# Kernel optimization log

Hardware: AMD Instinct MI355X
Metric: run time of the kernel (lower is better)

The kernel has to match this reference:

```python
import jax, jax.numpy as jnp
import numpy as np

N, E = 50000, 400000
HID, EDGE, NRBF = 128, 16, 32
CUTOFF = 5.0
EPS = 1e-8


def setup_inputs() -> dict:
    key = jax.random.key(0)
    ks = jax.random.split(key, 16)
    s = lambda fan_in: 1.0 / np.sqrt(fan_in)
    mlp_in = 3 * HID + NRBF + EDGE  # 432
    return {
        "h": jax.random.normal(ks[0], (N, HID), jnp.float32),
        "vec": jax.random.normal(ks[1], (N, 3, HID), jnp.float32),
        "coord": jax.random.normal(ks[2], (N, 3), jnp.float32),
        "edge_index": jax.random.randint(ks[3], (2, E), 0, N, jnp.int32),
        "edge_attr": jax.random.normal(ks[4], (E, EDGE), jnp.float32),
        "Wvp": jax.random.normal(ks[5], (HID, 3 * HID), jnp.float32) * s(HID),
        "W1": jax.random.normal(ks[6], (mlp_in, HID), jnp.float32) * s(mlp_in),
        "b1": jnp.zeros((HID,), jnp.float32),
        "W2": jax.random.normal(ks[7], (HID, HID), jnp.float32) * s(HID),
        "b2": jnp.zeros((HID,), jnp.float32),
        "W3": jax.random.normal(ks[8], (HID, 3 * HID), jnp.float32) * s(HID),
        "b3": jnp.zeros((3 * HID,), jnp.float32),
        "Wop": jax.random.normal(ks[9], (HID, 3 * HID), jnp.float32) * s(HID),
        "bop": jnp.zeros((3 * HID,), jnp.float32),
    }


def _rbf(d):
    # Gaussian smearing: centers on linspace(0, cutoff, n_rbf)
    offsets = jnp.linspace(0.0, CUTOFF, NRBF, dtype=d.dtype)
    coeff = -0.5 / (offsets[1] - offsets[0]) ** 2
    return jnp.exp(coeff * (d[:, None] - offsets) ** 2)  # [E, NRBF]


def reference(h, vec, coord, edge_index, edge_attr,
              Wvp, W1, b1, W2, b2, W3, b3, Wop, bop):
    row, col = edge_index[0], edge_index[1]
    x_ij = coord[row] - coord[col]                          # [E,3]
    d = jnp.sqrt(jnp.sum(x_ij * x_ij, axis=-1) + EPS)       # stable_norm
    d_ij = _rbf(d)                                          # [E,NRBF]

    vecp = jnp.einsum('nvh,hk->nvk', vec, Wvp)              # [N,3,3H]
    vec1, vec2, vec3 = jnp.split(vecp, 3, axis=-1)          # each [N,3,H]
    vec_dot = jnp.sum(vec1 * vec2, axis=1)                  # [N,H]

    cross = jnp.sum(vec1[row] * vec2[col], axis=1)          # [E,H]
    mlp_in = jnp.concatenate([h[row], h[col], d_ij, cross, edge_attr], axis=-1)
    x = jax.nn.silu(mlp_in @ W1 + b1)
    x = jax.nn.silu(x @ W2 + b2)
    msg = x @ W3 + b3                                       # [E,3H]
    msg_h, msg_v, msg_x = jnp.split(msg, 3, axis=1)

    h_aggr = jax.ops.segment_sum(msg_h, row, num_segments=N)           # [N,H]
    vec_msg = vec3[col] * msg_v[:, None, :] + msg_x[:, None, :] * x_ij[:, :, None]
    vec_aggr = jax.ops.segment_sum(vec_msg, row, num_segments=N)       # [N,3,H]

    o = h_aggr @ Wop + bop
    o1, o2, o3 = jnp.split(o, 3, axis=1)
    dh = vec_dot * o2 + o3
    dvec = vec3 * o1[:, None, :] + vec_aggr
    return dh, dvec
```

## Files before the change

### kernel.cpp

```cpp
#include <hip/hip_runtime.h>
#include <math.h>

constexpr int NN    = 50000;
constexpr int NE    = 400000;
constexpr int HID   = 128;

constexpr size_t OFF_VECP = 0;
constexpr size_t OFF_HAGG = 57600000;
constexpr size_t OFF_HW   = 64000000;
constexpr size_t OFF_OBUF = 64000000;
constexpr size_t OFF_WT   = 83200000;
constexpr size_t OFF_PERM = 83421184;
constexpr size_t OFF_DEG  = 83821184;
constexpr size_t OFF_CUR  = 83871184;
constexpr size_t WS_FLOATS = 83921184;

constexpr size_t O_HWH = 0;
constexpr size_t O_HWL = 32768;
constexpr size_t O_W1H = 65536;
constexpr size_t O_W1L = 90112;
constexpr size_t O_W2H = 114688;
constexpr size_t O_W2L = 131072;
constexpr size_t O_W3H = 147456;
constexpr size_t O_W3L = 196608;
constexpr size_t O_VPH = 245760;
constexpr size_t O_VPL = 294912;
constexpr size_t O_OPH = 344064;
constexpr size_t O_OPL = 393216;

typedef __attribute__((ext_vector_type(8))) short short8;
typedef __attribute__((ext_vector_type(4))) float f32x4;

__device__ __forceinline__ short f2bf_rne(float f) {
    unsigned u = __float_as_uint(f);
    u += 0x7fffu + ((u >> 16) & 1u);
    return (short)(u >> 16);
}
__device__ __forceinline__ float bf2f(short h) {
    return __uint_as_float(((unsigned)(unsigned short)h) << 16);
}
__device__ __forceinline__ void split8(const float* t, short8& ah, short8& al) {
#pragma unroll
    for (int j = 0; j < 8; ++j) {
        short hi = f2bf_rne(t[j]);
        ah[j] = hi;
        al[j] = f2bf_rne(t[j] - bf2f(hi));
    }
}
__device__ __forceinline__ f32x4 mfma3(short8 ah, short8 al, short8 bh, short8 bl, f32x4 c) {
    c = __builtin_amdgcn_mfma_f32_16x16x32_bf16(ah, bh, c, 0, 0, 0);
    c = __builtin_amdgcn_mfma_f32_16x16x32_bf16(al, bh, c, 0, 0, 0);
    c = __builtin_amdgcn_mfma_f32_16x16x32_bf16(ah, bl, c, 0, 0, 0);
    return c;
}

#define VLOAD8(dst, src) do { \
    *(float4*)&(dst)[0] = *(const float4*)(src); \
    *(float4*)&(dst)[4] = *(const float4*)((src) + 4); } while (0)

__global__ void sort_hist(const int* __restrict__ eidx, int* __restrict__ deg)
{
    int e = blockIdx.x * 256 + threadIdx.x;
    if (e < NE) atomicAdd(&deg[eidx[e]], 1);
}

__global__ void __launch_bounds__(1024)
sort_scan(const int* __restrict__ deg, int* __restrict__ cursor)
{
    __shared__ int part[1024];
    const int tid = threadIdx.x;
    const int base = tid * 49;
    int s = 0;
#pragma unroll 7
    for (int j = 0; j < 49; ++j) {
        int i = base + j;
        if (i < NN) s += deg[i];
    }
    part[tid] = s;
    __syncthreads();
    for (int off = 1; off < 1024; off <<= 1) {
        int v = (tid >= off) ? part[tid - off] : 0;
        __syncthreads();
        part[tid] += v;
        __syncthreads();
    }
    int run = part[tid] - s;
    for (int j = 0; j < 49; ++j) {
        int i = base + j;
        if (i < NN) { cursor[i] = run; run += deg[i]; }
    }
}

__global__ void sort_scatter(const int* __restrict__ eidx, int* __restrict__ cursor,
                             int* __restrict__ perm)
{
    int e = blockIdx.x * 256 + threadIdx.x;
    if (e < NE) {
        int pos = atomicAdd(&cursor[eidx[e]], 1);
        perm[pos] = e;
    }
}

__global__ void wprep_kernel(const float* __restrict__ W1, const float* __restrict__ W2,
                             const float* __restrict__ W3, const float* __restrict__ Wvp,
                             const float* __restrict__ Wop, short* __restrict__ wt)
{
    int idx = blockIdx.x * 256 + threadIdx.x;
    float v; size_t oh, ol;
    if (idx < 32768) {
        int j = idx >> 7, k = idx & 127;
        v = (j < 128) ? W1[(size_t)k * 128 + j] : W1[(size_t)(128 + k) * 128 + (j - 128)];
        oh = O_HWH + idx; ol = O_HWL + idx;
    } else if (idx < 57344) {
        int l = idx - 32768; int n = l / 192, k = l - n * 192;
        int r = (k < 128) ? (288 + k) : (k < 160) ? (256 + k - 128) : (k < 176) ? (416 + k - 160) : -1;
        v = (r < 0) ? 0.f : W1[(size_t)r * 128 + n];
        oh = O_W1H + l; ol = O_W1L + l;
    } else if (idx < 73728) {
        int l = idx - 57344; int n = l >> 7, k = l & 127;
        v = W2[(size_t)k * 128 + n];
        oh = O_W2H + l; ol = O_W2L + l;
    } else if (idx < 122880) {
        int l = idx - 73728; int n = l >> 7, k = l & 127;
        v = W3[(size_t)k * 384 + n];
        oh = O_W3H + l; ol = O_W3L + l;
    } else if (idx < 172032) {
        int l = idx - 122880; int n = l >> 7, k = l & 127;
        v = Wvp[(size_t)k * 384 + n];
        oh = O_VPH + l; ol = O_VPL + l;
    } else {
        int l = idx - 172032; int n = l >> 7, k = l & 127;
        v = Wop[(size_t)k * 384 + n];
        oh = O_OPH + l; ol = O_OPL + l;
    }
    short hi = f2bf_rne(v);
    wt[oh] = hi;
    wt[ol] = f2bf_rne(v - bf2f(hi));
}

template<int NT>
__global__ void __launch_bounds__(256, 3)
gemm_node(const float* __restrict__ A, int M,
          const short* __restrict__ wh, const short* __restrict__ wl,
          float* __restrict__ C, const float* __restrict__ bias)
{
    const int N = NT * 64;
    const int tid = threadIdx.x, wave = tid >> 6, lane = tid & 63;
    const int m = lane & 15, kg = lane >> 4;
    const int gm0 = blockIdx.x * 32;
    const int nb = wave * NT * 16;
    const f32x4 zf = {0.f, 0.f, 0.f, 0.f};
    f32x4 acc[2][NT];
#pragma unroll
    for (int mt = 0; mt < 2; ++mt)
#pragma unroll
        for (int tt = 0; tt < NT; ++tt) acc[mt][tt] = zf;

    for (int ks = 0; ks < 4; ++ks) {
        short8 ah[2], al[2];
#pragma unroll
        for (int mt = 0; mt < 2; ++mt) {
            int r = gm0 + mt * 16 + m;
            if (r >= M) r = M - 1;
            float tmp[8];
            VLOAD8(tmp, A + (size_t)r * 128 + ks * 32 + kg * 8);
            split8(tmp, ah[mt], al[mt]);
        }
#pragma unroll
        for (int tt = 0; tt < NT; ++tt) {
            size_t wo = (size_t)(nb + tt * 16 + m) * 128 + ks * 32 + kg * 8;
            short8 bh = *(const short8*)(wh + wo);
            short8 bl = *(const short8*)(wl + wo);
#pragma unroll
            for (int mt = 0; mt < 2; ++mt)
                acc[mt][tt] = mfma3(ah[mt], al[mt], bh, bl, acc[mt][tt]);
        }
    }
    float bv[NT];
#pragma unroll
    for (int tt = 0; tt < NT; ++tt) bv[tt] = bias ? bias[nb + tt * 16 + m] : 0.f;
#pragma unroll
    for (int mt = 0; mt < 2; ++mt)
#pragma unroll
        for (int r = 0; r < 4; ++r) {
            int row = gm0 + mt * 16 + kg * 4 + r;
            if (row < M) {
#pragma unroll
                for (int tt = 0; tt < NT; ++tt)
                    C[(size_t)row * N + nb + tt * 16 + m] = acc[mt][tt][r] + bv[tt];
            }
        }
}

__global__ void prep_kernel(float* __restrict__ hagg, float* __restrict__ dvec)
{
    int idx = blockIdx.x * 256 + threadIdx.x;
    int n = idx >> 7, k = idx & 127;
    hagg[idx] = 0.f;
    size_t db = (size_t)n * 384 + k;
    dvec[db] = 0.f; dvec[db + 128] = 0.f; dvec[db + 256] = 0.f;
}

__global__ void fin_kernel(const float* __restrict__ vecp, const float* __restrict__ obuf,
                           float* __restrict__ dh, float* __restrict__ dvec)
{
    int idx = blockIdx.x * 256 + threadIdx.x;
    int n = idx >> 7, k = idx & 127;
    size_t b = (size_t)n * 1152;
    float vd = vecp[b + k]       * vecp[b + 128 + k]
             + vecp[b + 384 + k] * vecp[b + 512 + k]
             + vecp[b + 768 + k] * vecp[b + 896 + k];
    const float* o = obuf + (size_t)n * 384;
    float o1 = o[k], o2 = o[128 + k], o3 = o[256 + k];
    dh[idx] = vd * o2 + o3;
    size_t vb = b + 256 + k;
    size_t db = (size_t)n * 384 + k;
    dvec[db]       += vecp[vb]       * o1;
    dvec[db + 128] += vecp[vb + 384] * o1;
    dvec[db + 256] += vecp[vb + 768] * o1;
}

__global__ void __launch_bounds__(256, 3)
edge_kernel(const float* __restrict__ vecp, const float* __restrict__ hw,
            const float* __restrict__ coord, const int* __restrict__ eidx,
            const float* __restrict__ eattr, const short* __restrict__ wt,
            const int* __restrict__ perm,
            const float* __restrict__ b1, const float* __restrict__ b2,
            const float* __restrict__ b3,
            float* __restrict__ hagg, float* __restrict__ dvec)
{
    __shared__ __align__(16) short abh[64][40];
    __shared__ __align__(16) short abl[64][40];
    __shared__ __align__(16) short xh[64][136];
    __shared__ __align__(16) short xl[64][136];
    __shared__ int   s_row[64], s_col[64], s_es[64];
    __shared__ float s_xij[64][3];
    __shared__ float s_d[64];

    const int tid = threadIdx.x;
    const int wave = tid >> 6, lane = tid & 63;
    const int m = lane & 15, kg = lane >> 4;
    const int nb = wave * 32;
    const int eb = blockIdx.x * 64;
    const int be = tid >> 2;
    const int bq = (tid & 3) * 8;

    if (tid < 64) {
        int es = perm[eb + tid];
        int r = eidx[es], c = eidx[NE + es];
        s_es[tid] = es; s_row[tid] = r; s_col[tid] = c;
        float x0 = coord[r * 3 + 0] - coord[c * 3 + 0];
        float x1 = coord[r * 3 + 1] - coord[c * 3 + 1];
        float x2 = coord[r * 3 + 2] - coord[c * 3 + 2];
        s_xij[tid][0] = x0; s_xij[tid][1] = x1; s_xij[tid][2] = x2;
        s_d[tid] = sqrtf(x0 * x0 + x1 * x1 + x2 * x2 + 1e-8f);
    }
    __syncthreads();

    const f32x4 zf = {0.f, 0.f, 0.f, 0.f};
    const float delta = 5.0f / 31.0f;
    const float coeff = -0.5f / (delta * delta);
    const int brow = s_row[be], bcol = s_col[be], bes = s_es[be];

    float pA[8], pB[8], pC[8], pD[8], pE[8], pF[8];
    auto issue = [&](int ks) {
        if (ks < 4) {
            int kk = ks * 32 + bq;
            const float* vr = vecp + (size_t)brow * 1152 + kk;
            const float* vc = vecp + (size_t)bcol * 1152 + 128 + kk;
            VLOAD8(pA, vr);       VLOAD8(pB, vc);
            VLOAD8(pC, vr + 384); VLOAD8(pD, vc + 384);
            VLOAD8(pE, vr + 768); VLOAD8(pF, vc + 768);
        } else if (ks == 5) {
            if (bq < 16) VLOAD8(pA, eattr + (size_t)bes * 16 + bq);
        }
    };
    auto commit = [&](int ks) {
        float tmp[8];
        if (ks < 4) {
#pragma unroll
            for (int j = 0; j < 8; ++j)
                tmp[j] = pA[j] * pB[j] + pC[j] * pD[j] + pE[j] * pF[j];
        } else if (ks == 4) {
            float dd = s_d[be];
#pragma unroll
            for (int j = 0; j < 8; ++j) {
                float x = dd - (float)(bq + j) * delta;
                tmp[j] = __expf(coeff * x * x);
            }
        } else {
#pragma unroll
            for (int j = 0; j < 8; ++j) tmp[j] = (bq < 16) ? pA[j] : 0.f;
        }
        short8 sh, sl; split8(tmp, sh, sl);
        *(short8*)&abh[be][bq] = sh;
        *(short8*)&abl[be][bq] = sl;
    };

    f32x4 acc[4][2];
#pragma unroll
    for (int mt = 0; mt < 4; ++mt) { acc[mt][0] = zf; acc[mt][1] = zf; }

    issue(0); commit(0);
    __syncthreads();
    for (int ks = 0; ks < 6; ++ks) {
        if (ks < 5) issue(ks + 1);
        short8 ah4[4], al4[4];
#pragma unroll
        for (int mt = 0; mt < 4; ++mt) {
            ah4[mt] = *(const short8*)&abh[mt * 16 + m][kg * 8];
            al4[mt] = *(const short8*)&abl[mt * 16 + m][kg * 8];
        }
#pragma unroll
        for (int tt = 0; tt < 2; ++tt) {
            size_t wo = (size_t)(nb + tt * 16 + m) * 192 + ks * 32 + kg * 8;
            short8 bh = *(const short8*)(wt + O_W1H + wo);
            short8 bl = *(const short8*)(wt + O_W1L + wo);
#pragma unroll
            for (int mt = 0; mt < 4; ++mt)
                acc[mt][tt] = mfma3(ah4[mt], al4[mt], bh, bl, acc[mt][tt]);
        }
        __syncthreads();
        if (ks < 5) { commit(ks + 1); __syncthreads(); }
    }

    {
        float b1v[2] = { b1[nb + m], b1[nb + 16 + m] };
#pragma unroll
        for (int mt = 0; mt < 4; ++mt)
#pragma unroll
            for (int r = 0; r < 4; ++r) {
                int e = mt * 16 + kg * 4 + r;
                const float* hr = hw + (size_t)s_row[e] * 256;
                const float* hc = hw + (size_t)s_col[e] * 256 + 128;
#pragma unroll
                for (int tt = 0; tt < 2; ++tt) {
                    int n = nb + tt * 16 + m;
                    float v = acc[mt][tt][r] + hr[n] + hc[n] + b1v[tt];
                    float sv = v * __builtin_amdgcn_rcpf(1.f + __expf(-v));
                    short hi = f2bf_rne(sv);
                    xh[e][n] = hi;
                    xl[e][n] = f2bf_rne(sv - bf2f(hi));
                }
            }
    }
    __syncthreads();

#pragma unroll
    for (int mt = 0; mt < 4; ++mt) { acc[mt][0] = zf; acc[mt][1] = zf; }
    for (int ks = 0; ks < 4; ++ks) {
        short8 ah4[4], al4[4];
#pragma unroll
        for (int mt = 0; mt < 4; ++mt) {
            ah4[mt] = *(const short8*)&xh[mt * 16 + m][ks * 32 + kg * 8];
            al4[mt] = *(const short8*)&xl[mt * 16 + m][ks * 32 + kg * 8];
        }
#pragma unroll
        for (int tt = 0; tt < 2; ++tt) {
            size_t wo = (size_t)(nb + tt * 16 + m) * 128 + ks * 32 + kg * 8;
            short8 bh = *(const short8*)(wt + O_W2H + wo);
            short8 bl = *(const short8*)(wt + O_W2L + wo);
#pragma unroll
            for (int mt = 0; mt < 4; ++mt)
                acc[mt][tt] = mfma3(ah4[mt], al4[mt], bh, bl, acc[mt][tt]);
        }
    }
    {
        float b2v[2] = { b2[nb + m], b2[nb + 16 + m] };
#pragma unroll
        for (int mt = 0; mt < 4; ++mt)
#pragma unroll
            for (int tt = 0; tt < 2; ++tt)
#pragma unroll
                for (int r = 0; r < 4; ++r) {
                    float v = acc[mt][tt][r] + b2v[tt];
                    acc[mt][tt][r] = v * __builtin_amdgcn_rcpf(1.f + __expf(-v));
                }
    }
    __syncthreads();
#pragma unroll
    for (int mt = 0; mt < 4; ++mt)
#pragma unroll
        for (int tt = 0; tt < 2; ++tt)
#pragma unroll
            for (int r = 0; r < 4; ++r) {
                int e = mt * 16 + kg * 4 + r;
                int n = nb + tt * 16 + m;
                float sv = acc[mt][tt][r];
                short hi = f2bf_rne(sv);
                xh[e][n] = hi;
                xl[e][n] = f2bf_rne(sv - bf2f(hi));
            }
    __syncthreads();

    float msgv[4][2][4];
    for (int c = 0; c < 3; ++c) {
        f32x4 a3[4][2];
#pragma unroll
        for (int mt = 0; mt < 4; ++mt) { a3[mt][0] = zf; a3[mt][1] = zf; }
        for (int ks = 0; ks < 4; ++ks) {
            short8 ah4[4], al4[4];
#pragma unroll
            for (int mt = 0; mt < 4; ++mt) {
                ah4[mt] = *(const short8*)&xh[mt * 16 + m][ks * 32 + kg * 8];
                al4[mt] = *(const short8*)&xl[mt * 16 + m][ks * 32 + kg * 8];
            }
#pragma unroll
            for (int tt = 0; tt < 2; ++tt) {
                size_t wo = (size_t)(c * 128 + nb + tt * 16 + m) * 128 + ks * 32 + kg * 8;
                short8 bh = *(const short8*)(wt + O_W3H + wo);
                short8 bl = *(const short8*)(wt + O_W3L + wo);
#pragma unroll
                for (int mt = 0; mt < 4; ++mt)
                    a3[mt][tt] = mfma3(ah4[mt], al4[mt], bh, bl, a3[mt][tt]);
            }
        }
        float bv[2] = { b3[c * 128 + nb + m], b3[c * 128 + nb + 16 + m] };
        const int n0 = nb + m, n1 = nb + 16 + m;
        if (c == 0) {
            int cur = s_row[kg * 4];
            float s0 = 0.f, s1 = 0.f;
#pragma unroll
            for (int mt = 0; mt < 4; ++mt)
#pragma unroll
                for (int r = 0; r < 4; ++r) {
                    int rr = s_row[mt * 16 + kg * 4 + r];
                    float v0 = a3[mt][0][r] + bv[0];
                    float v1 = a3[mt][1][r] + bv[1];
                    if (rr != cur) {
                        atomicAdd(&hagg[(size_t)cur * 128 + n0], s0);
                        atomicAdd(&hagg[(size_t)cur * 128 + n1], s1);
                        cur = rr; s0 = 0.f; s1 = 0.f;
                    }
                    s0 += v0; s1 += v1;
                }
            atomicAdd(&hagg[(size_t)cur * 128 + n0], s0);
            atomicAdd(&hagg[(size_t)cur * 128 + n1], s1);
        } else if (c == 1) {
#pragma unroll
            for (int mt = 0; mt < 4; ++mt)
#pragma unroll
                for (int tt = 0; tt < 2; ++tt)
#pragma unroll
                    for (int r = 0; r < 4; ++r)
                        msgv[mt][tt][r] = a3[mt][tt][r] + bv[tt];
        } else {
            int cur = s_row[kg * 4];
            float sd[6] = {0.f, 0.f, 0.f, 0.f, 0.f, 0.f};
#pragma unroll
            for (int mt = 0; mt < 4; ++mt)
#pragma unroll
                for (int r = 0; r < 4; ++r) {
                    int e = mt * 16 + kg * 4 + r;
                    int rr = s_row[e];
                    if (rr != cur) {
                        float* dst = dvec + (size_t)cur * 384;
                        atomicAdd(dst + n0,       sd[0]);
                        atomicAdd(dst + 128 + n0, sd[1]);
                        atomicAdd(dst + 256 + n0, sd[2]);
                        atomicAdd(dst + n1,       sd[3]);
                        atomicAdd(dst + 128 + n1, sd[4]);
                        atomicAdd(dst + 256 + n1, sd[5]);
                        cur = rr;
#pragma unroll
                        for (int q = 0; q < 6; ++q) sd[q] = 0.f;
                    }
                    const float* v3 = vecp + (size_t)s_col[e] * 1152 + 256;
                    const float xj0 = s_xij[e][0], xj1 = s_xij[e][1], xj2 = s_xij[e][2];
                    float mx0 = a3[mt][0][r] + bv[0], mx1 = a3[mt][1][r] + bv[1];
                    float mv0 = msgv[mt][0][r],       mv1 = msgv[mt][1][r];
                    sd[0] += v3[n0]       * mv0 + xj0 * mx0;
                    sd[1] += v3[384 + n0] * mv0 + xj1 * mx0;
                    sd[2] += v3[768 + n0] * mv0 + xj2 * mx0;
                    sd[3] += v3[n1]       * mv1 + xj0 * mx1;
                    sd[4] += v3[384 + n1] * mv1 + xj1 * mx1;
                    sd[5] += v3[768 + n1] * mv1 + xj2 * mx1;
                }
            float* dst = dvec + (size_t)cur * 384;
            atomicAdd(dst + n0,       sd[0]);
            atomicAdd(dst + 128 + n0, sd[1]);
            atomicAdd(dst + 256 + n0, sd[2]);
            atomicAdd(dst + n1,       sd[3]);
            atomicAdd(dst + 128 + n1, sd[4]);
            atomicAdd(dst + 256 + n1, sd[5]);
        }
    }
}

extern "C" void kernel_launch(void* const* d_in, const int* in_sizes, int n_in,
                              void* d_out, int out_size, void* d_ws, size_t ws_size,
                              hipStream_t stream)
{
    const float* h     = (const float*)d_in[0];
    const float* vec   = (const float*)d_in[1];
    const float* coord = (const float*)d_in[2];
    const int*   eidx  = (const int*)  d_in[3];
    const float* eattr = (const float*)d_in[4];
    const float* Wvp   = (const float*)d_in[5];
    const float* W1    = (const float*)d_in[6];
    const float* b1    = (const float*)d_in[7];
    const float* W2    = (const float*)d_in[8];
    const float* b2    = (const float*)d_in[9];
    const float* W3    = (const float*)d_in[10];
    const float* b3    = (const float*)d_in[11];
    const float* Wop   = (const float*)d_in[12];
    const float* bop   = (const float*)d_in[13];

    if (ws_size < WS_FLOATS * sizeof(float)) return;

    float* ws   = (float*)d_ws;
    float* vecp = ws + OFF_VECP;
    float* hagg = ws + OFF_HAGG;
    float* hw   = ws + OFF_HW;
    float* obuf = ws + OFF_OBUF;
    short* wt   = (short*)(ws + OFF_WT);
    int*   perm = (int*)(ws + OFF_PERM);
    int*   deg  = (int*)(ws + OFF_DEG);
    int*   cur  = (int*)(ws + OFF_CUR);
    float* dh   = (float*)d_out;
    float* dvec = (float*)d_out + (size_t)NN * HID;

    dim3 b256(256);
    hipMemsetAsync(deg, 0, NN * sizeof(int), stream);
    sort_hist<<<1563, b256, 0, stream>>>(eidx, deg);
    sort_scan<<<1, 1024, 0, stream>>>(deg, cur);
    sort_scatter<<<1563, b256, 0, stream>>>(eidx, cur, perm);
    wprep_kernel<<<864, b256, 0, stream>>>(W1, W2, W3, Wvp, Wop, wt);
    gemm_node<6><<<4688, b256, 0, stream>>>(vec, 150000, wt + O_VPH, wt + O_VPL, vecp, nullptr);
    gemm_node<4><<<1563, b256, 0, stream>>>(h, 50000, wt + O_HWH, wt + O_HWL, hw, nullptr);
    prep_kernel<<<25000, b256, 0, stream>>>(hagg, dvec);
    edge_kernel<<<6250, b256, 0, stream>>>(vecp, hw, coord, eidx, eattr, wt, perm,
                                           b1, b2, b3, hagg, dvec);
    gemm_node<6><<<1563, b256, 0, stream>>>(hagg, 50000, wt + O_OPH, wt + O_OPL, obuf, bop);
    fin_kernel<<<25000, b256, 0, stream>>>(vecp, obuf, dh, dvec);
}
```

Before: 1.363 ms.

## Fuse setup kernels, fuse output GEMM with finalize, alias edge LDS buffers

Merges histogram, weight prep and zero-init into one misc kernel, and fuses the output projection GEMM with the finalize step so obuf is never written or re-read. The edge kernel aliases its LDS staging buffers to cut shared memory and raises launch bounds to 4 blocks per SM. It also batches gathered hw and vec3 loads ahead of their use so more memory requests are in flight. Risks include register pressure from the higher occupancy target and from the prefetch arrays, and correctness depends on abh/xh aliasing being separated by barriers.

```diff
diff --git a/kernel.cpp b/kernel.cpp
--- a/kernel.cpp
+++ b/kernel.cpp
@@ -8,7 +8,6 @@
 constexpr size_t OFF_VECP = 0;
 constexpr size_t OFF_HAGG = 57600000;
 constexpr size_t OFF_HW   = 64000000;
-constexpr size_t OFF_OBUF = 64000000;
 constexpr size_t OFF_WT   = 83200000;
 constexpr size_t OFF_PERM = 83421184;
 constexpr size_t OFF_DEG  = 83821184;
@@ -58,10 +57,54 @@
     *(float4*)&(dst)[0] = *(const float4*)(src); \
     *(float4*)&(dst)[4] = *(const float4*)((src) + 4); } while (0)
 
-__global__ void sort_hist(const int* __restrict__ eidx, int* __restrict__ deg)
-{
-    int e = blockIdx.x * 256 + threadIdx.x;
-    if (e < NE) atomicAdd(&deg[eidx[e]], 1);
+__global__ void misc_kernel(const float* __restrict__ W1, const float* __restrict__ W2,
+                            const float* __restrict__ W3, const float* __restrict__ Wvp,
+                            const float* __restrict__ Wop, short* __restrict__ wt,
+                            const int* __restrict__ eidx, int* __restrict__ deg,
+                            float* __restrict__ hagg, float* __restrict__ dvec)
+{
+    const int bid = blockIdx.x;
+    const int idx = bid * 256 + threadIdx.x;
+    {
+        int n = idx >> 7, k = idx & 127;
+        hagg[idx] = 0.f;
+        size_t db = (size_t)n * 384 + k;
+        dvec[db] = 0.f; dvec[db + 128] = 0.f; dvec[db + 256] = 0.f;
+    }
+    if (bid < 864) {
+        float v; size_t oh, ol;
+        if (idx < 32768) {
+            int j = idx >> 7, k = idx & 127;
+            v = (j < 128) ? W1[(size_t)k * 128 + j] : W1[(size_t)(128 + k) * 128 + (j - 128)];
+            oh = O_HWH + idx; ol = O_HWL + idx;
+        } else if (idx < 57344) {
+            int l = idx - 32768; int n = l / 192, k = l - n * 192;
+            int r = (k < 128) ? (288 + k) : (k < 160) ? (256 + k - 128) : (k < 176) ? (416 + k - 160) : -1;
+            v = (r < 0) ? 0.f : W1[(size_t)r * 128 + n];
+            oh = O_W1H + l; ol = O_W1L + l;
+        } else if (idx < 73728) {
+            int l = idx - 57344; int n = l >> 7, k = l & 127;
+            v = W2[(size_t)k * 128 + n];
+            oh = O_W2H + l; ol = O_W2L + l;
+        } else if (idx < 122880) {
+            int l = idx - 73728; int n = l >> 7, k = l & 127;
+            v = W3[(size_t)k * 384 + n];
+            oh = O_W3H + l; ol = O_W3L + l;
+        } else if (idx < 172032) {
+            int l = idx - 122880; int n = l >> 7, k = l & 127;
+            v = Wvp[(size_t)k * 384 + n];
+            oh = O_VPH + l; ol = O_VPL + l;
+        } else {
+            int l = idx - 172032; int n = l >> 7, k = l & 127;
+            v = Wop[(size_t)k * 384 + n];
+            oh = O_OPH + l; ol = O_OPL + l;
+        }
+        short hi = f2bf_rne(v);
+        wt[oh] = hi;
+        wt[ol] = f2bf_rne(v - bf2f(hi));
+    }
+    if (bid < 1563 && idx < NE)
+        atomicAdd(&deg[eidx[idx]], 1);
 }
 
 __global__ void __launch_bounds__(1024)
@@ -101,43 +144,6 @@
     }
 }
 
-__global__ void wprep_kernel(const float* __restrict__ W1, const float* __restrict__ W2,
-                             const float* __restrict__ W3, const float* __restrict__ Wvp,
-                             const float* __restrict__ Wop, short* __restrict__ wt)
-{
-    int idx = blockIdx.x * 256 + threadIdx.x;
-    float v; size_t oh, ol;
-    if (idx < 32768) {
-        int j = idx >> 7, k = idx & 127;
-        v = (j < 128) ? W1[(size_t)k * 128 + j] : W1[(size_t)(128 + k) * 128 + (j - 128)];
-        oh = O_HWH + idx; ol = O_HWL + idx;
-    } else if (idx < 57344) {
-        int l = idx - 32768; int n = l / 192, k = l - n * 192;
-        int r = (k < 128) ? (288 + k) : (k < 160) ? (256 + k - 128) : (k < 176) ? (416 + k - 160) : -1;
-        v = (r < 0) ? 0.f : W1[(size_t)r * 128 + n];
-        oh = O_W1H + l; ol = O_W1L + l;
-    } else if (idx < 73728) {
-        int l = idx - 57344; int n = l >> 7, k = l & 127;
-        v = W2[(size_t)k * 128 + n];
-        oh = O_W2H + l; ol = O_W2L + l;
-    } else if (idx < 122880) {
-        int l = idx - 73728; int n = l >> 7, k = l & 127;
-        v = W3[(size_t)k * 384 + n];
-        oh = O_W3H + l; ol = O_W3L + l;
-    } else if (idx < 172032) {
-        int l = idx - 122880; int n = l >> 7, k = l & 127;
-        v = Wvp[(size_t)k * 384 + n];
-        oh = O_VPH + l; ol = O_VPL + l;
-    } else {
-        int l = idx - 172032; int n = l >> 7, k = l & 127;
-        v = Wop[(size_t)k * 384 + n];
-        oh = O_OPH + l; ol = O_OPL + l;
-    }
-    short hi = f2bf_rne(v);
-    wt[oh] = hi;
-    wt[ol] = f2bf_rne(v - bf2f(hi));
-}
-
 template<int NT>
 __global__ void __launch_bounds__(256, 3)
 gemm_node(const float* __restrict__ A, int M,
@@ -192,35 +198,77 @@
         }
 }
 
-__global__ void prep_kernel(float* __restrict__ hagg, float* __restrict__ dvec)
-{
-    int idx = blockIdx.x * 256 + threadIdx.x;
-    int n = idx >> 7, k = idx & 127;
-    hagg[idx] = 0.f;
-    size_t db = (size_t)n * 384 + k;
-    dvec[db] = 0.f; dvec[db + 128] = 0.f; dvec[db + 256] = 0.f;
-}
-
-__global__ void fin_kernel(const float* __restrict__ vecp, const float* __restrict__ obuf,
-                           float* __restrict__ dh, float* __restrict__ dvec)
-{
-    int idx = blockIdx.x * 256 + threadIdx.x;
-    int n = idx >> 7, k = idx & 127;
-    size_t b = (size_t)n * 1152;
-    float vd = vecp[b + k]       * vecp[b + 128 + k]
-             + vecp[b + 384 + k] * vecp[b + 512 + k]
-             + vecp[b + 768 + k] * vecp[b + 896 + k];
-    const float* o = obuf + (size_t)n * 384;
-    float o1 = o[k], o2 = o[128 + k], o3 = o[256 + k];
-    dh[idx] = vd * o2 + o3;
-    size_t vb = b + 256 + k;
-    size_t db = (size_t)n * 384 + k;
-    dvec[db]       += vecp[vb]       * o1;
-    dvec[db + 128] += vecp[vb + 384] * o1;
-    dvec[db + 256] += vecp[vb + 768] * o1;
-}
-
 __global__ void __launch_bounds__(256, 3)
+gemm_fin(const float* __restrict__ hagg, const float* __restrict__ vecp,
+         const short* __restrict__ wh, const short* __restrict__ wl,
+         const float* __restrict__ bop, float* __restrict__ dh,
+         float* __restrict__ dvec, int M)
+{
+    const int tid = threadIdx.x, wave = tid >> 6, lane = tid & 63;
+    const int m = lane & 15, kg = lane >> 4;
+    const int gm0 = blockIdx.x * 32;
+    const int nb = wave * 32;
+    const f32x4 zf = {0.f, 0.f, 0.f, 0.f};
+    f32x4 acc[2][6];
+#pragma unroll
+    for (int mt = 0; mt < 2; ++mt)
+#pragma unroll
+        for (int t = 0; t < 6; ++t) acc[mt][t] = zf;
+
+    for (int ks = 0; ks < 4; ++ks) {
+        short8 ah[2], al[2];
+#pragma unroll
+        for (int mt = 0; mt < 2; ++mt) {
+            int r = gm0 + mt * 16 + m;
+            if (r >= M) r = M - 1;
+            float tmp[8];
+            VLOAD8(tmp, hagg + (size_t)r * 128 + ks * 32 + kg * 8);
+            split8(tmp, ah[mt], al[mt]);
+        }
+#pragma unroll
+        for (int seg = 0; seg < 3; ++seg)
+#pragma unroll
+            for (int tt = 0; tt < 2; ++tt) {
+                size_t wo = (size_t)(seg * 128 + nb + tt * 16 + m) * 128 + ks * 32 + kg * 8;
+                short8 bh = *(const short8*)(wh + wo);
+                short8 bl = *(const short8*)(wl + wo);
+#pragma unroll
+                for (int mt = 0; mt < 2; ++mt)
+                    acc[mt][seg * 2 + tt] = mfma3(ah[mt], al[mt], bh, bl, acc[mt][seg * 2 + tt]);
+            }
+    }
+    float bo[3][2];
+#pragma unroll
+    for (int seg = 0; seg < 3; ++seg)
+#pragma unroll
+        for (int tt = 0; tt < 2; ++tt) bo[seg][tt] = bop[seg * 128 + nb + tt * 16 + m];
+
+#pragma unroll
+    for (int mt = 0; mt < 2; ++mt)
+#pragma unroll
+        for (int r = 0; r < 4; ++r) {
+            int row = gm0 + mt * 16 + kg * 4 + r;
+            if (row >= M) continue;
+            size_t b = (size_t)row * 1152;
+#pragma unroll
+            for (int tt = 0; tt < 2; ++tt) {
+                int k = nb + tt * 16 + m;
+                float o1 = acc[mt][0 * 2 + tt][r] + bo[0][tt];
+                float o2 = acc[mt][1 * 2 + tt][r] + bo[1][tt];
+                float o3 = acc[mt][2 * 2 + tt][r] + bo[2][tt];
+                float vd = vecp[b + k]       * vecp[b + 128 + k]
+                         + vecp[b + 384 + k] * vecp[b + 512 + k]
+                         + vecp[b + 768 + k] * vecp[b + 896 + k];
+                dh[(size_t)row * 128 + k] = vd * o2 + o3;
+                size_t db = (size_t)row * 384 + k;
+                dvec[db]       += vecp[b + 256 + k]  * o1;
+                dvec[db + 128] += vecp[b + 640 + k]  * o1;
+                dvec[db + 256] += vecp[b + 1024 + k] * o1;
+            }
+        }
+}
+
+__global__ void __launch_bounds__(256, 4)
 edge_kernel(const float* __restrict__ vecp, const float* __restrict__ hw,
             const float* __restrict__ coord, const int* __restrict__ eidx,
             const float* __restrict__ eattr, const short* __restrict__ wt,
@@ -229,10 +277,11 @@
             const float* __restrict__ b3,
             float* __restrict__ hagg, float* __restrict__ dvec)
 {
-    __shared__ __align__(16) short abh[64][40];
-    __shared__ __align__(16) short abl[64][40];
-    __shared__ __align__(16) short xh[64][136];
-    __shared__ __align__(16) short xl[64][136];
+    __shared__ __align__(16) unsigned char smem[34816];
+    short (*abh)[40]  = (short(*)[40])(&smem[0]);
+    short (*abl)[40]  = (short(*)[40])(&smem[5120]);
+    short (*xh)[136]  = (short(*)[136])(&smem[0]);
+    short (*xl)[136]  = (short(*)[136])(&smem[17408]);
     __shared__ int   s_row[64], s_col[64], s_es[64];
     __shared__ float s_xij[64][3];
     __shared__ float s_d[64];
@@ -327,22 +376,30 @@
     {
         float b1v[2] = { b1[nb + m], b1[nb + 16 + m] };
 #pragma unroll
-        for (int mt = 0; mt < 4; ++mt)
+        for (int mt = 0; mt < 4; ++mt) {
+            float hb[4][4];
 #pragma unroll
             for (int r = 0; r < 4; ++r) {
                 int e = mt * 16 + kg * 4 + r;
                 const float* hr = hw + (size_t)s_row[e] * 256;
                 const float* hc = hw + (size_t)s_col[e] * 256 + 128;
+                hb[r][0] = hr[nb + m];      hb[r][1] = hc[nb + m];
+                hb[r][2] = hr[nb + 16 + m]; hb[r][3] = hc[nb + 16 + m];
+            }
+#pragma unroll
+            for (int r = 0; r < 4; ++r) {
+                int e = mt * 16 + kg * 4 + r;
 #pragma unroll
                 for (int tt = 0; tt < 2; ++tt) {
                     int n = nb + tt * 16 + m;
-                    float v = acc[mt][tt][r] + hr[n] + hc[n] + b1v[tt];
+                    float v = acc[mt][tt][r] + hb[r][tt * 2] + hb[r][tt * 2 + 1] + b1v[tt];
                     float sv = v * __builtin_amdgcn_rcpf(1.f + __expf(-v));
                     short hi = f2bf_rne(sv);
                     xh[e][n] = hi;
                     xl[e][n] = f2bf_rne(sv - bf2f(hi));
                 }
             }
+        }
     }
     __syncthreads();
 
@@ -448,7 +505,15 @@
             int cur = s_row[kg * 4];
             float sd[6] = {0.f, 0.f, 0.f, 0.f, 0.f, 0.f};
 #pragma unroll
-            for (int mt = 0; mt < 4; ++mt)
+            for (int mt = 0; mt < 4; ++mt) {
+                float v3b[4][6];
+#pragma unroll
+                for (int r = 0; r < 4; ++r) {
+                    int e = mt * 16 + kg * 4 + r;
+                    const float* v3 = vecp + (size_t)s_col[e] * 1152 + 256;
+                    v3b[r][0] = v3[n0]; v3b[r][1] = v3[384 + n0]; v3b[r][2] = v3[768 + n0];
+                    v3b[r][3] = v3[n1]; v3b[r][4] = v3[384 + n1]; v3b[r][5] = v3[768 + n1];
+                }
 #pragma unroll
                 for (int r = 0; r < 4; ++r) {
                     int e = mt * 16 + kg * 4 + r;
@@ -465,17 +530,17 @@
 #pragma unroll
                         for (int q = 0; q < 6; ++q) sd[q] = 0.f;
                     }
-                    const float* v3 = vecp + (size_t)s_col[e] * 1152 + 256;
                     const float xj0 = s_xij[e][0], xj1 = s_xij[e][1], xj2 = s_xij[e][2];
                     float mx0 = a3[mt][0][r] + bv[0], mx1 = a3[mt][1][r] + bv[1];
                     float mv0 = msgv[mt][0][r],       mv1 = msgv[mt][1][r];
-                    sd[0] += v3[n0]       * mv0 + xj0 * mx0;
-                    sd[1] += v3[384 + n0] * mv0 + xj1 * mx0;
-                    sd[2] += v3[768 + n0] * mv0 + xj2 * mx0;
-                    sd[3] += v3[n1]       * mv1 + xj0 * mx1;
-                    sd[4] += v3[384 + n1] * mv1 + xj1 * mx1;
-                    sd[5] += v3[768 + n1] * mv1 + xj2 * mx1;
+                    sd[0] += v3b[r][0] * mv0 + xj0 * mx0;
+                    sd[1] += v3b[r][1] * mv0 + xj1 * mx0;
+                    sd[2] += v3b[r][2] * mv0 + xj2 * mx0;
+                    sd[3] += v3b[r][3] * mv1 + xj0 * mx1;
+                    sd[4] += v3b[r][4] * mv1 + xj1 * mx1;
+                    sd[5] += v3b[r][5] * mv1 + xj2 * mx1;
                 }
+            }
             float* dst = dvec + (size_t)cur * 384;
             atomicAdd(dst + n0,       sd[0]);
             atomicAdd(dst + 128 + n0, sd[1]);
@@ -512,7 +577,6 @@
     float* vecp = ws + OFF_VECP;
     float* hagg = ws + OFF_HAGG;
     float* hw   = ws + OFF_HW;
-    float* obuf = ws + OFF_OBUF;
     short* wt   = (short*)(ws + OFF_WT);
     int*   perm = (int*)(ws + OFF_PERM);
     int*   deg  = (int*)(ws + OFF_DEG);
@@ -522,15 +586,12 @@
 
     dim3 b256(256);
     hipMemsetAsync(deg, 0, NN * sizeof(int), stream);
-    sort_hist<<<1563, b256, 0, stream>>>(eidx, deg);
+    misc_kernel<<<25000, b256, 0, stream>>>(W1, W2, W3, Wvp, Wop, wt, eidx, deg, hagg, dvec);
     sort_scan<<<1, 1024, 0, stream>>>(deg, cur);
     sort_scatter<<<1563, b256, 0, stream>>>(eidx, cur, perm);
-    wprep_kernel<<<864, b256, 0, stream>>>(W1, W2, W3, Wvp, Wop, wt);
     gemm_node<6><<<4688, b256, 0, stream>>>(vec, 150000, wt + O_VPH, wt + O_VPL, vecp, nullptr);
     gemm_node<4><<<1563, b256, 0, stream>>>(h, 50000, wt + O_HWH, wt + O_HWL, hw, nullptr);
-    prep_kernel<<<25000, b256, 0, stream>>>(hagg, dvec);
     edge_kernel<<<6250, b256, 0, stream>>>(vecp, hw, coord, eidx, eattr, wt, perm,
                                            b1, b2, b3, hagg, dvec);
-    gemm_node<6><<<1563, b256, 0, stream>>>(hagg, 50000, wt + O_OPH, wt + O_OPL, obuf, bop);
-    fin_kernel<<<25000, b256, 0, stream>>>(vecp, obuf, dh, dvec);
-}
+    gemm_fin<<<1563, b256, 0, stream>>>(hagg, vecp, wt + O_OPH, wt + O_OPL, bop, dh, dvec, 50000);
+}
```

Measured after the change: 1.313 ms. 3.7% less time.
